# Kernel tuning notes

Measured on AMD Instinct MI355X. Metric: run time of the kernel, lower is better.

The kernel has to match this reference:

```python
import jax, jax.numpy as jnp
import numpy as np

N, E, G = 100000, 800000, 4096
H, F_NODE, F_EDGE, T_OUT = 256, 133, 7, 12
NUM_LAYERS, NUM_TIMESTEPS = 4, 2
SLOPE = 0.01  # negative_slope used throughout AttentiveFP


def _lrelu(v):
    return jax.nn.leaky_relu(v, SLOPE)


def _seg_softmax(logits, seg, n):
    # PyG softmax: exp(x - segment_max) / (segment_sum + 1e-16)
    m = jax.ops.segment_max(logits, seg, num_segments=n)
    e = jnp.exp(logits - m[seg])
    s = jax.ops.segment_sum(e, seg, num_segments=n)
    return e / (s[seg] + 1e-16)


def _gru(xin, h, w_ih, w_hh, b_ih, b_hh):
    # torch.nn.GRUCell, gate order (r, z, n)
    gi = xin @ w_ih.T + b_ih
    gh = h @ w_hh.T + b_hh
    i_r, i_z, i_n = jnp.split(gi, 3, axis=-1)
    h_r, h_z, h_n = jnp.split(gh, 3, axis=-1)
    r = jax.nn.sigmoid(i_r + h_r)
    z = jax.nn.sigmoid(i_z + h_z)
    n = jnp.tanh(i_n + r * h_n)
    return (1.0 - z) * n + z * h


def setup_inputs() -> dict:
    key = jax.random.key(0)
    ks = iter(jax.random.split(key, 40))
    rn = lambda shape, s=0.1: jax.random.normal(next(ks), shape, jnp.float32) * s
    return {
        'x': jax.random.normal(next(ks), (N, F_NODE), jnp.float32),
        'edge_attr': jax.random.normal(next(ks), (E, F_EDGE), jnp.float32),
        'lin1_w': rn((H, F_NODE)), 'lin1_b': rn((H,)),
        'gate_att_l': rn((H,)), 'gate_att_r': rn((H,)),
        'gate_lin1_w': rn((H, H + F_EDGE)), 'gate_lin2_w': rn((H, H)), 'gate_bias': rn((H,)),
        'atom_lin_w': rn((NUM_LAYERS - 1, H, H)), 'atom_att_src': rn((NUM_LAYERS - 1, H)),
        'atom_att_dst': rn((NUM_LAYERS - 1, H)), 'atom_bias': rn((NUM_LAYERS - 1, H)),
        'gru_w_ih': rn((NUM_LAYERS, 3 * H, H)), 'gru_w_hh': rn((NUM_LAYERS, 3 * H, H)),
        'gru_b_ih': rn((NUM_LAYERS, 3 * H)), 'gru_b_hh': rn((NUM_LAYERS, 3 * H)),
        'mol_lin_w': rn((H, H)), 'mol_att_src': rn((H,)), 'mol_att_dst': rn((H,)), 'mol_bias': rn((H,)),
        'mol_gru_w_ih': rn((3 * H, H)), 'mol_gru_w_hh': rn((3 * H, H)),
        'mol_gru_b_ih': rn((3 * H,)), 'mol_gru_b_hh': rn((3 * H,)),
        'lin2_w': rn((H, H)), 'lin2_b': rn((H,)),
        'fc_w': rn((T_OUT, H)), 'fc_b': rn((T_OUT,)),
        'edge_index': jax.random.randint(next(ks), (2, E), 0, N),
        'batch': jnp.sort(jax.random.randint(next(ks), (N,), 0, G)),
        'num_graphs': G,
    }


def reference(x, edge_attr, lin1_w, lin1_b, gate_att_l, gate_att_r, gate_lin1_w,
              gate_lin2_w, gate_bias, atom_lin_w, atom_att_src, atom_att_dst, atom_bias,
              gru_w_ih, gru_w_hh, gru_b_ih, gru_b_hh, mol_lin_w, mol_att_src, mol_att_dst,
              mol_bias, mol_gru_w_ih, mol_gru_w_hh, mol_gru_b_ih, mol_gru_b_hh,
              lin2_w, lin2_b, fc_w, fc_b, edge_index, batch, num_graphs):
    # Eval mode: all dropouts are identity.
    src, dst = edge_index[0], edge_index[1]
    n = x.shape[0]

    x0 = _lrelu(x @ lin1_w.T + lin1_b)  # [N, H]

    # --- GATEConv: edge-feature attention message passing ---
    xj = _lrelu(jnp.concatenate([x0[src], edge_attr], axis=-1) @ gate_lin1_w.T)  # [E, H]
    alpha = _lrelu(xj @ gate_att_l + (x0 @ gate_att_r)[dst])
    alpha = _seg_softmax(alpha, dst, n)
    msg = (x0 @ gate_lin2_w.T)[src] * alpha[:, None]  # [E, H]
    h = jax.ops.segment_sum(msg, dst, num_segments=n) + gate_bias
    xcur = jax.nn.relu(_gru(jax.nn.elu(h), x0, gru_w_ih[0], gru_w_hh[0], gru_b_ih[0], gru_b_hh[0]))

    # --- (num_layers-1) GATConv layers (heads=1, no self loops, slope 0.01) ---
    for l in range(atom_lin_w.shape[0]):
        xl = xcur @ atom_lin_w[l].T  # [N, H]
        a = _lrelu((xl @ atom_att_src[l])[src] + (xl @ atom_att_dst[l])[dst])
        a = _seg_softmax(a, dst, n)
        h = jax.ops.segment_sum(xl[src] * a[:, None], dst, num_segments=n) + atom_bias[l]
        xcur = jax.nn.relu(_gru(jax.nn.elu(h), xcur,
                                gru_w_ih[l + 1], gru_w_hh[l + 1], gru_b_ih[l + 1], gru_b_hh[l + 1]))

    # --- Molecule embedding: attention pooling over node->graph bipartite edges ---
    out = jax.nn.relu(jax.ops.segment_sum(xcur, batch, num_segments=num_graphs))  # [G, H]
    xm = xcur @ mol_lin_w.T              # src transform, fixed across timesteps
    a_src = xm @ mol_att_src             # [N]
    for _ in range(NUM_TIMESTEPS):
        a = _lrelu(a_src + ((out @ mol_lin_w.T) @ mol_att_dst)[batch])
        a = _seg_softmax(a, batch, num_graphs)
        h = jax.ops.segment_sum(xm * a[:, None], batch, num_segments=num_graphs) + mol_bias
        out = jax.nn.relu(_gru(jax.nn.elu(h), out,
                               mol_gru_w_ih, mol_gru_w_hh, mol_gru_b_ih, mol_gru_b_hh))

    emb = out @ lin2_w.T + lin2_b        # AttentiveFP lin2
    return emb @ fc_w.T + fc_b           # [G, num_tasks]
```

## Files before the change

### kernel.cpp

```cpp
#include <hip/hip_runtime.h>
#include <math.h>
#include <stdio.h>
#include <stdint.h>

#define NH 256
#define NH3 768
#define FNODE 133
#define FEDGE 7
#define LDW_GATE1 263
#define NGRAPH 4096
#define NTASK 12
#define SLOPE 0.01f
#define CHUNK 25000
#define PADK 40
#define KPAD_X 160
#define LDC2 512
#define SCAN_TILE 2048

typedef __attribute__((ext_vector_type(4))) float f32x4;
typedef __attribute__((ext_vector_type(8))) _Float16 f16x8;
typedef __attribute__((ext_vector_type(4))) _Float16 f16x4;
typedef __attribute__((ext_vector_type(2))) _Float16 f16x2;

static __device__ __forceinline__ float lrelu_f(float x) { return x > 0.f ? x : SLOPE * x; }
static __device__ __forceinline__ f16x2 lrelu2(f16x2 v) {
    f16x2 z = {(_Float16)0.f, (_Float16)0.f};
    f16x2 s = {(_Float16)SLOPE, (_Float16)SLOPE};
    return __builtin_elementwise_max(v, z) + __builtin_elementwise_min(v, z) * s;
}

template<int ACT, int OB, int AF16>
static __device__ __forceinline__ void gemm_core(
    _Float16* As, _Float16* Ws,
    const void* __restrict__ Av, const float* __restrict__ W,
    const float* __restrict__ bias, const float* __restrict__ bias2,
    void* __restrict__ Cout,
    int M, int K, int Nout, int ldA, int ldW, int ldC, int ocol, int Kw, int bn)
{
    const int bm = blockIdx.y * 64;
    const int tid = threadIdx.x;
    const int wv = tid >> 6, lane = tid & 63;
    const int l15 = lane & 15, l4 = lane >> 4;
    const bool kvec = ((K & 31) == 0) && ((ldA & 3) == 0);
    const bool wvec = ((K & 31) == 0) && ((ldW & 3) == 0) && (Kw == K);
    const int ar = tid >> 2, akq = (tid & 3) * 8;

    f32x4 acc[16];
#pragma unroll
    for (int c = 0; c < 16; ++c) acc[c] = (f32x4){0.f, 0.f, 0.f, 0.f};

    for (int k0 = 0; k0 < K; k0 += 32) {
        {
            const int ga = bm + ar;
            _Float16* dstA = &As[ar * PADK + akq];
            if (AF16) {
                const _Float16* A = (const _Float16*)Av;
                if (ga < M) {
                    *reinterpret_cast<f16x8*>(dstA) =
                        *reinterpret_cast<const f16x8*>(A + (size_t)ga * ldA + k0 + akq);
                } else {
#pragma unroll
                    for (int j = 0; j < 8; ++j) dstA[j] = (_Float16)0.f;
                }
            } else {
                const float* A = (const float*)Av;
                if (ga < M && kvec) {
                    const float4* ap4 = reinterpret_cast<const float4*>(A + (size_t)ga * ldA + k0 + akq);
                    float4 v0 = ap4[0], v1 = ap4[1];
                    dstA[0] = (_Float16)v0.x; dstA[1] = (_Float16)v0.y;
                    dstA[2] = (_Float16)v0.z; dstA[3] = (_Float16)v0.w;
                    dstA[4] = (_Float16)v1.x; dstA[5] = (_Float16)v1.y;
                    dstA[6] = (_Float16)v1.z; dstA[7] = (_Float16)v1.w;
                } else {
                    const float* ap = A + (size_t)ga * ldA + k0 + akq;
#pragma unroll
                    for (int j = 0; j < 8; ++j) {
                        int gk = k0 + akq + j;
                        float v = (ga < M && gk < K) ? ap[j] : 0.f;
                        dstA[j] = (_Float16)v;
                    }
                }
            }
        }
#pragma unroll
        for (int q = 0; q < 4; ++q) {
            const int r = ar + 64 * q;
            const int gw = bn + r;
            _Float16* dstW = &Ws[r * PADK + akq];
            if (gw < Nout && wvec) {
                const float4* wp4 = reinterpret_cast<const float4*>(W + (size_t)gw * ldW + k0 + akq);
                float4 v0 = wp4[0], v1 = wp4[1];
                dstW[0] = (_Float16)v0.x; dstW[1] = (_Float16)v0.y;
                dstW[2] = (_Float16)v0.z; dstW[3] = (_Float16)v0.w;
                dstW[4] = (_Float16)v1.x; dstW[5] = (_Float16)v1.y;
                dstW[6] = (_Float16)v1.z; dstW[7] = (_Float16)v1.w;
            } else {
                const float* wp = W + (size_t)gw * ldW + k0 + akq;
#pragma unroll
                for (int j = 0; j < 8; ++j) {
                    int gk = k0 + akq + j;
                    float v = (gw < Nout && gk < Kw) ? wp[j] : 0.f;
                    dstW[j] = (_Float16)v;
                }
            }
        }
        __syncthreads();
        f16x8 af = *reinterpret_cast<const f16x8*>(&As[(wv * 16 + l15) * PADK + l4 * 8]);
#pragma unroll
        for (int c = 0; c < 16; ++c) {
            f16x8 wf = *reinterpret_cast<const f16x8*>(&Ws[(c * 16 + l15) * PADK + l4 * 8]);
            acc[c] = __builtin_amdgcn_mfma_f32_16x16x32_f16(af, wf, acc[c], 0, 0, 0);
        }
        __syncthreads();
    }

#pragma unroll
    for (int c = 0; c < 16; ++c) {
        int gc = bn + c * 16 + l15;
        if (gc >= Nout) continue;
        float bv = (bias ? bias[gc] : 0.f) + (bias2 ? bias2[gc] : 0.f);
#pragma unroll
        for (int q = 0; q < 4; ++q) {
            int gr = bm + wv * 16 + l4 * 4 + q;
            if (gr >= M) continue;
            float v = acc[c][q] + bv;
            if (ACT == 1) v = lrelu_f(v);
            else if (ACT == 2) v = (v > 0.f ? v : expm1f(v));
            else if (ACT == 3) v = 1.f / (1.f + expf(-v));
            size_t off = (size_t)gr * ldC + ocol + gc;
            if (OB) ((_Float16*)Cout)[off] = (_Float16)v;
            else    ((float*)Cout)[off] = v;
        }
    }
}

template<int ACT, int OB, int AF16>
__global__ __launch_bounds__(256, 4) void gemm_mfma(
    const void* __restrict__ A, const float* __restrict__ W,
    const float* __restrict__ bias, void* __restrict__ Cout,
    int M, int K, int Nout, int ldA, int ldW, int ldC, int ocol, int Kw)
{
    __shared__ _Float16 As[64 * PADK];
    __shared__ _Float16 Ws[256 * PADK];
    gemm_core<ACT, OB, AF16>(As, Ws, A, W, bias, nullptr, Cout,
                             M, K, Nout, ldA, ldW, ldC, ocol, Kw, blockIdx.x * 256);
}

__global__ __launch_bounds__(256, 4) void gemm_gru_a(
    const _Float16* __restrict__ Acat, const float* __restrict__ wcat,
    const float* __restrict__ wih, const float* __restrict__ bih, const float* __restrict__ bhh,
    _Float16* __restrict__ srz, _Float16* __restrict__ innb, int mc)
{
    __shared__ _Float16 As[64 * PADK];
    __shared__ _Float16 Ws[256 * PADK];
    int z = blockIdx.z;
    if (z < 2)
        gemm_core<3, 1, 1>(As, Ws, Acat, wcat, bih, bhh, srz,
                           mc, 512, 512, LDC2, 512, 512, 0, 512, z * 256);
    else
        gemm_core<0, 1, 1>(As, Ws, Acat, wih + 512 * NH, bih + 512, nullptr, innb,
                           mc, NH, NH, LDC2, NH, NH, 0, NH, 0);
}

__global__ __launch_bounds__(256, 4) void gemm_gru_b(
    _Float16* __restrict__ Acat, const float* __restrict__ whh, const float* __restrict__ bhh,
    const _Float16* __restrict__ srz, const _Float16* __restrict__ innb,
    const float* __restrict__ us, const float* __restrict__ ud,
    float* __restrict__ dotr, float* __restrict__ adst, int mc)
{
    __shared__ _Float16 As[64 * PADK];
    __shared__ _Float16 Ws[256 * PADK];
    const float* Wn = whh + 512 * NH;
    const int bm = blockIdx.y * 64;
    const int tid = threadIdx.x;
    const int wv = tid >> 6, lane = tid & 63;
    const int l15 = lane & 15, l4 = lane >> 4;
    const int ar = tid >> 2, akq = (tid & 3) * 8;

    f32x4 acc[16];
#pragma unroll
    for (int c = 0; c < 16; ++c) acc[c] = (f32x4){0.f, 0.f, 0.f, 0.f};

    for (int k0 = 0; k0 < NH; k0 += 32) {
        {
            const int ga = bm + ar;
            _Float16* dstA = &As[ar * PADK + akq];
            if (ga < mc) {
                *reinterpret_cast<f16x8*>(dstA) =
                    *reinterpret_cast<const f16x8*>(Acat + (size_t)ga * LDC2 + NH + k0 + akq);
            } else {
#pragma unroll
                for (int j = 0; j < 8; ++j) dstA[j] = (_Float16)0.f;
            }
        }
#pragma unroll
        for (int q = 0; q < 4; ++q) {
            const int r = ar + 64 * q;
            _Float16* dstW = &Ws[r * PADK + akq];
            const float4* wp4 = reinterpret_cast<const float4*>(Wn + (size_t)r * NH + k0 + akq);
            float4 v0 = wp4[0], v1 = wp4[1];
            dstW[0] = (_Float16)v0.x; dstW[1] = (_Float16)v0.y;
            dstW[2] = (_Float16)v0.z; dstW[3] = (_Float16)v0.w;
            dstW[4] = (_Float16)v1.x; dstW[5] = (_Float16)v1.y;
            dstW[6] = (_Float16)v1.z; dstW[7] = (_Float16)v1.w;
        }
        __syncthreads();
        f16x8 af = *reinterpret_cast<const f16x8*>(&As[(wv * 16 + l15) * PADK + l4 * 8]);
#pragma unroll
        for (int c = 0; c < 16; ++c) {
            f16x8 wf = *reinterpret_cast<const f16x8*>(&Ws[(c * 16 + l15) * PADK + l4 * 8]);
            acc[c] = __builtin_amdgcn_mfma_f32_16x16x32_f16(af, wf, acc[c], 0, 0, 0);
        }
        __syncthreads();
    }

    float pd1[4] = {0.f, 0.f, 0.f, 0.f};
    float pd2[4] = {0.f, 0.f, 0.f, 0.f};
#pragma unroll
    for (int c = 0; c < 16; ++c) {
        int gc = c * 16 + l15;
        float bhn = bhh[512 + gc];
        float usv = us ? us[gc] : 0.f;
        float udv = ud ? ud[gc] : 0.f;
#pragma unroll
        for (int q = 0; q < 4; ++q) {
            int gr = bm + wv * 16 + l4 * 4 + q;
            if (gr >= mc) continue;
            float hn = acc[c][q] + bhn;
            float rr = (float)srz[(size_t)gr * 512 + gc];
            float zz = (float)srz[(size_t)gr * 512 + 256 + gc];
            float inn = (float)innb[(size_t)gr * NH + gc];
            float nn = tanhf(inn + rr * hn);
            size_t xoff = (size_t)gr * LDC2 + NH + gc;
            float xold = (float)Acat[xoff];
            float hv = fmaxf((1.f - zz) * nn + zz * xold, 0.f);
            Acat[xoff] = (_Float16)hv;
            pd1[q] += hv * usv;
            pd2[q] += hv * udv;
        }
    }
    if (us) {
#pragma unroll
        for (int off = 1; off < 16; off <<= 1) {
#pragma unroll
            for (int q = 0; q < 4; ++q) {
                pd1[q] += __shfl_xor(pd1[q], off);
                pd2[q] += __shfl_xor(pd2[q], off);
            }
        }
        if (l15 == 0) {
#pragma unroll
            for (int q = 0; q < 4; ++q) {
                int gr = bm + wv * 16 + l4 * 4 + q;
                if (gr < mc) {
                    dotr[gr] = pd1[q];
                    if (ud) adst[gr] = pd2[q];
                }
            }
        }
    }
}

template<int ACT, int OB>
__global__ __launch_bounds__(256, 4) void gemm_mfma2(
    const float* __restrict__ A0, const float* __restrict__ A1,
    const float* __restrict__ W0, const float* __restrict__ W1,
    void* __restrict__ C0, void* __restrict__ C1, int M, int K, int Nout)
{
    __shared__ _Float16 As[64 * PADK];
    __shared__ _Float16 Ws[256 * PADK];
    int bn = blockIdx.x * 256;
    if (blockIdx.z == 0)
        gemm_core<ACT, OB, 0>(As, Ws, A0, W0, nullptr, nullptr, C0, M, K, Nout, K, K, Nout, 0, K, bn);
    else
        gemm_core<ACT, OB, 0>(As, Ws, A1, W1, nullptr, nullptr, C1, M, K, Nout, K, K, Nout, 0, K, bn);
}

__global__ void build_wcat(const float* __restrict__ wih, const float* __restrict__ whh,
                           float* __restrict__ wcat)
{
    int i = blockIdx.x * 256 + threadIdx.x;
    if (i >= 512 * 512) return;
    int j = i >> 9, k = i & 511;
    wcat[i] = (k < 256) ? wih[j * 256 + k] : whh[j * 256 + (k - 256)];
}

__global__ void pad_cast_f16(const float* __restrict__ in, _Float16* __restrict__ out,
                             int M, int Kin, int Kout)
{
    size_t i = (size_t)blockIdx.x * 256 + threadIdx.x;
    if (i >= (size_t)M * Kout) return;
    int r = (int)(i / Kout), k = (int)(i % Kout);
    out[i] = (k < Kin) ? (_Float16)in[(size_t)r * Kin + k] : (_Float16)0.f;
}

__global__ __launch_bounds__(256) void gemm_nt(
    const float* __restrict__ A, const float* __restrict__ W,
    const float* __restrict__ bias, float* __restrict__ C,
    int M, int K, int Nout, int ldW, int act)
{
    __shared__ float As[16][65];
    __shared__ float Ws[16][65];
    const int bm = blockIdx.y * 64;
    const int bn = blockIdx.x * 64;
    const int tid = threadIdx.x;
    const int tr = tid >> 4, tc = tid & 15;
    const int lrow = tid >> 2, lk = (tid & 3) * 4;
    float acc[4][4] = {};
    for (int k0 = 0; k0 < K; k0 += 16) {
#pragma unroll
        for (int j = 0; j < 4; ++j) {
            int gk = k0 + lk + j;
            int ga = bm + lrow;
            As[lk + j][lrow] = (ga < M && gk < K) ? A[(size_t)ga * K + gk] : 0.f;
            int gw = bn + lrow;
            Ws[lk + j][lrow] = (gw < Nout && gk < K) ? W[(size_t)gw * ldW + gk] : 0.f;
        }
        __syncthreads();
#pragma unroll
        for (int kk = 0; kk < 16; ++kk) {
            float av[4], bv[4];
#pragma unroll
            for (int i = 0; i < 4; ++i) av[i] = As[kk][tr * 4 + i];
#pragma unroll
            for (int i = 0; i < 4; ++i) bv[i] = Ws[kk][tc * 4 + i];
#pragma unroll
            for (int i = 0; i < 4; ++i)
#pragma unroll
                for (int j = 0; j < 4; ++j) acc[i][j] += av[i] * bv[j];
        }
        __syncthreads();
    }
#pragma unroll
    for (int i = 0; i < 4; ++i) {
        int m = bm + tr * 4 + i;
        if (m >= M) continue;
#pragma unroll
        for (int j = 0; j < 4; ++j) {
            int n = bn + tc * 4 + j;
            if (n >= Nout) continue;
            float v = acc[i][j];
            if (bias) v += bias[n];
            if (act == 1) v = lrelu_f(v);
            C[(size_t)m * Nout + n] = v;
        }
    }
}

__global__ void zero_i32(int* p, int n) {
    int i = blockIdx.x * 256 + threadIdx.x;
    if (i < n) p[i] = 0;
}
__global__ void hist_k(const int* __restrict__ key, int* __restrict__ deg, int E) {
    int i = blockIdx.x * 256 + threadIdx.x;
    if (i < E) atomicAdd(&deg[key[i]], 1);
}
__global__ __launch_bounds__(256) void scan_pass1(
    const int* __restrict__ deg, int* __restrict__ bsum, int Nn)
{
    __shared__ int lds[256];
    int b = blockIdx.x, t = threadIdx.x;
    int base = b * SCAN_TILE + t * 8;
    int s = 0;
#pragma unroll
    for (int q = 0; q < 8; ++q) { int i = base + q; if (i < Nn) s += deg[i]; }
    lds[t] = s;
    __syncthreads();
    for (int off = 128; off; off >>= 1) {
        if (t < off) lds[t] += lds[t + off];
        __syncthreads();
    }
    if (t == 0) bsum[b] = lds[0];
}
__global__ __launch_bounds__(256) void scan_pass2(
    const int* __restrict__ bsum, int* __restrict__ boff, int nb, int* __restrict__ total)
{
    __shared__ int lds[256];
    int t = threadIdx.x;
    int v = (t < nb) ? bsum[t] : 0;
    lds[t] = v;
    __syncthreads();
    for (int off = 1; off < 256; off <<= 1) {
        int u = (t >= off) ? lds[t - off] : 0;
        __syncthreads();
        lds[t] += u;
        __syncthreads();
    }
    if (t < nb) boff[t] = lds[t] - v;
    if (t == 255 && total) *total = lds[255];
}
__global__ __launch_bounds__(256) void scan_pass3(
    const int* __restrict__ deg, const int* __restrict__ boff,
    int* __restrict__ rowptr, int* __restrict__ cursor, int Nn)
{
    __shared__ int lds[256];
    int b = blockIdx.x, t = threadIdx.x;
    int base = b * SCAN_TILE + t * 8;
    int v[8];
    int s = 0;
#pragma unroll
    for (int q = 0; q < 8; ++q) { int i = base + q; v[q] = (i < Nn) ? deg[i] : 0; s += v[q]; }
    lds[t] = s;
    __syncthreads();
    for (int off = 1; off < 256; off <<= 1) {
        int u = (t >= off) ? lds[t - off] : 0;
        __syncthreads();
        lds[t] += u;
        __syncthreads();
    }
    int run = boff[b] + lds[t] - s;
#pragma unroll
    for (int q = 0; q < 8; ++q) {
        int i = base + q;
        if (i < Nn) { rowptr[i] = run; cursor[i] = run; run += v[q]; }
    }
}
__global__ void csr_scatter(const int* __restrict__ src, const int* __restrict__ dst,
                            int* __restrict__ cursor, int* __restrict__ esrc,
                            int* __restrict__ pos, int E)
{
    int e = blockIdx.x * 256 + threadIdx.x;
    if (e < E) {
        int p = atomicAdd(&cursor[dst[e]], 1);
        esrc[p] = src[e];
        pos[e] = p;
    }
}
__global__ void csc_scatter(const int* __restrict__ src, int* __restrict__ cursor,
                            int* __restrict__ seid, int E)
{
    int e = blockIdx.x * 256 + threadIdx.x;
    if (e < E) {
        int p = atomicAdd(&cursor[src[e]], 1);
        seid[p] = e;
    }
}
__global__ void edge_csc_build(const float* __restrict__ edge_attr, const int* __restrict__ seid,
// ... 167 lines not shown
    float a0 = 0.f, a1 = 0.f, a2 = 0.f, a3 = 0.f;
    if (beg < end) {
        float dg = ddot[g];
        float m = -3.4e38f;
        for (int i = beg + lane; i < end; i += 64)
            m = fmaxf(m, lrelu_f(dotr[i] + dg));
#pragma unroll
        for (int off = 32; off; off >>= 1) m = fmaxf(m, __shfl_xor(m, off));
        float s = 0.f;
        for (int i = beg + lane; i < end; i += 64)
            s += expf(lrelu_f(dotr[i] + dg) - m);
#pragma unroll
        for (int off = 32; off; off >>= 1) s += __shfl_xor(s, off);
        float inv = 1.f / (s + 1e-16f);
        for (int i = beg; i < end; ++i) {
            float a = expf(lrelu_f(dotr[i] + dg) - m) * inv;
            const _Float16* xr = X + (size_t)i * ldX;
            a0 += a * (float)xr[lane];       a1 += a * (float)xr[64 + lane];
            a2 += a * (float)xr[128 + lane]; a3 += a * (float)xr[192 + lane];
        }
    }
    float* hr = hout + (size_t)g * NH;
    hr[lane] = a0; hr[64 + lane] = a1; hr[128 + lane] = a2; hr[192 + lane] = a3;
}

__global__ __launch_bounds__(256) void graph_sum_relu(
    const _Float16* __restrict__ X, int ldX, const int* __restrict__ gptr,
    float* __restrict__ out, int G)
{
    int wv = threadIdx.x >> 6, lane = threadIdx.x & 63;
    int g = blockIdx.x * 4 + wv;
    if (g >= G) return;
    int beg = gptr[g], end = gptr[g + 1];
    float a0 = 0.f, a1 = 0.f, a2 = 0.f, a3 = 0.f;
    for (int i = beg; i < end; ++i) {
        const _Float16* xr = X + (size_t)i * ldX;
        a0 += (float)xr[lane];       a1 += (float)xr[64 + lane];
        a2 += (float)xr[128 + lane]; a3 += (float)xr[192 + lane];
    }
    float* hr = out + (size_t)g * NH;
    hr[lane] = fmaxf(a0, 0.f); hr[64 + lane] = fmaxf(a1, 0.f);
    hr[128 + lane] = fmaxf(a2, 0.f); hr[192 + lane] = fmaxf(a3, 0.f);
}

template<typename TX>
__global__ __launch_bounds__(256) void node_dot(
    const TX* __restrict__ X, int ldX, const float* __restrict__ v1, const float* __restrict__ v2,
    float* __restrict__ o1, float* __restrict__ o2, int M)
{
    __shared__ float s1[NH], s2[NH];
    int tid = threadIdx.x;
    s1[tid] = v1[tid];
    s2[tid] = v2 ? v2[tid] : 0.f;
    __syncthreads();
    int wv = tid >> 6, lane = tid & 63;
    for (int n = blockIdx.x * 4 + wv; n < M; n += gridDim.x * 4) {
        float a1 = 0.f, a2 = 0.f;
#pragma unroll
        for (int i = 0; i < 4; ++i) {
            int hh = i * 64 + lane;
            float xv = (float)X[(size_t)n * ldX + hh];
            a1 += xv * s1[hh];
            a2 += xv * s2[hh];
        }
#pragma unroll
        for (int off = 32; off; off >>= 1) { a1 += __shfl_xor(a1, off); a2 += __shfl_xor(a2, off); }
        if (lane == 0) { o1[n] = a1; if (o2) o2[n] = a2; }
    }
}

__global__ __launch_bounds__(256) void matvec_left(
    const float* __restrict__ Wm, const float* __restrict__ a, float* __restrict__ v)
{
    int j = threadIdx.x;
    float s = 0.f;
    for (int i = 0; i < NH; ++i) s += a[i] * Wm[(size_t)i * NH + j];
    v[j] = s;
}

__global__ __launch_bounds__(256) void gru_combine(
    const _Float16* __restrict__ gi, const _Float16* __restrict__ gh,
    const float* __restrict__ b_ih, const float* __restrict__ b_hh,
    const float* __restrict__ hprev, float* __restrict__ out, int M)
{
    size_t t = (size_t)blockIdx.x * 256 + threadIdx.x;
    if (t >= (size_t)M * 32) return;
    int n = (int)(t >> 5), j0 = ((int)t & 31) * 8;
    size_t b3 = (size_t)n * NH3;
    f16x8 vir = *reinterpret_cast<const f16x8*>(&gi[b3 + j0]);
    f16x8 viz = *reinterpret_cast<const f16x8*>(&gi[b3 + NH + j0]);
    f16x8 vin = *reinterpret_cast<const f16x8*>(&gi[b3 + 2 * NH + j0]);
    f16x8 vhr = *reinterpret_cast<const f16x8*>(&gh[b3 + j0]);
    f16x8 vhz = *reinterpret_cast<const f16x8*>(&gh[b3 + NH + j0]);
    f16x8 vhn = *reinterpret_cast<const f16x8*>(&gh[b3 + 2 * NH + j0]);
    size_t hb = (size_t)n * NH + j0;
#pragma unroll
    for (int q = 0; q < 8; ++q) {
        int j = j0 + q;
        float r = 1.f / (1.f + expf(-((float)vir[q] + b_ih[j] + (float)vhr[q] + b_hh[j])));
        float z = 1.f / (1.f + expf(-((float)viz[q] + b_ih[NH + j] + (float)vhz[q] + b_hh[NH + j])));
        float nn = tanhf((float)vin[q] + b_ih[2 * NH + j] + r * ((float)vhn[q] + b_hh[2 * NH + j]));
        out[hb + q] = fmaxf((1.f - z) * nn + z * hprev[hb + q], 0.f);
    }
}

extern "C" void kernel_launch(void* const* d_in, const int* in_sizes, int n_in,
                              void* d_out, int out_size, void* d_ws, size_t ws_size,
                              hipStream_t stream)
{
    const float* x          = (const float*)d_in[0];
    const float* edge_attr  = (const float*)d_in[1];
    const float* lin1_w     = (const float*)d_in[2];
    const float* lin1_b     = (const float*)d_in[3];
    const float* gate_att_l = (const float*)d_in[4];
    const float* gate_att_r = (const float*)d_in[5];
    const float* gate_lin1_w= (const float*)d_in[6];
    const float* gate_lin2_w= (const float*)d_in[7];
    const float* gate_bias  = (const float*)d_in[8];
    const float* atom_lin_w = (const float*)d_in[9];
    const float* atom_att_src=(const float*)d_in[10];
    const float* atom_att_dst=(const float*)d_in[11];
    const float* atom_bias  = (const float*)d_in[12];
    const float* gru_w_ih   = (const float*)d_in[13];
    const float* gru_w_hh   = (const float*)d_in[14];
    const float* gru_b_ih   = (const float*)d_in[15];
    const float* gru_b_hh   = (const float*)d_in[16];
    const float* mol_lin_w  = (const float*)d_in[17];
    const float* mol_att_src= (const float*)d_in[18];
    const float* mol_att_dst= (const float*)d_in[19];
    const float* mol_bias   = (const float*)d_in[20];
    const float* mol_gru_w_ih=(const float*)d_in[21];
    const float* mol_gru_w_hh=(const float*)d_in[22];
    const float* mol_gru_b_ih=(const float*)d_in[23];
    const float* mol_gru_b_hh=(const float*)d_in[24];
    const float* lin2_w     = (const float*)d_in[25];
    const float* lin2_b     = (const float*)d_in[26];
    const float* fc_w       = (const float*)d_in[27];
    const float* fc_b       = (const float*)d_in[28];
    const int*   edge_index = (const int*)d_in[29];
    const int*   batch      = (const int*)d_in[30];

    const int N = in_sizes[0] / FNODE;
    const int E = in_sizes[1] / FEDGE;
    const int G = NGRAPH;
    const int* src = edge_index;
    const int* dst = edge_index + E;

    float* w = (float*)d_ws;
    size_t o = 0;
    auto alloc = [&](size_t cnt) { size_t r = o; o += cnt; return r; };
    const size_t o_B1cat = alloc((size_t)N * NH);
    const size_t o_B2    = alloc((size_t)N * NH / 2);
    const size_t o_B3    = alloc((size_t)CHUNK * 512);
    const size_t o_wcat  = alloc((size_t)512 * 512);
    const size_t o_elog  = alloc((size_t)E);
    const size_t o_dotr  = alloc((size_t)N);
    const size_t o_adst  = alloc((size_t)N);
    const size_t o_ddot  = alloc((size_t)G);
    const size_t o_vvec  = alloc((size_t)NH);
    const size_t o_usrc  = alloc((size_t)NH);
    const size_t o_udst  = alloc((size_t)NH);
    const size_t o_rowp  = alloc((size_t)N + 1);
    const size_t o_srowp = alloc((size_t)N + 1);
    const size_t o_deg   = alloc((size_t)N);
    const size_t o_curs  = alloc((size_t)N);
    const size_t o_bsum  = alloc((size_t)512);
    const size_t o_esrc  = alloc((size_t)E);
    const size_t o_pos   = alloc((size_t)E);
    const size_t o_seid  = alloc((size_t)E);
    const size_t o_ecsc  = alloc((size_t)E * 4);
    const size_t o_pcsc  = alloc((size_t)E);
    const size_t o_gptr  = alloc((size_t)G + 1);
    if (o * sizeof(float) > ws_size) {
        fprintf(stderr, "kernel_launch: ws too small: need %zu have %zu\n", o * 4, ws_size);
        return;
    }

    _Float16* B1cat = (_Float16*)(w + o_B1cat);
    _Float16* xcur  = B1cat + NH;
    _Float16* B2 = (_Float16*)(w + o_B2);
    float* B3   = w + o_B3;
    float* wcat = w + o_wcat;
    float* elog = w + o_elog;
    float* dotr = w + o_dotr;
    float* adst = w + o_adst;
    float* ddot = w + o_ddot;
    float* vvec = w + o_vvec;
    float* usrc = w + o_usrc;
    float* udst = w + o_udst;
    int* rowptr  = (int*)(w + o_rowp);
    int* srowptr = (int*)(w + o_srowp);
    int* deg     = (int*)(w + o_deg);
    int* cursor  = (int*)(w + o_curs);
    int* bsum    = (int*)(w + o_bsum);
    int* boff    = bsum + 256;
    int* esrc    = (int*)(w + o_esrc);
    int* pos     = (int*)(w + o_pos);
    int* seid    = (int*)(w + o_seid);
    _Float16* ecsc = (_Float16*)(w + o_ecsc);
    int* pcsc    = (int*)(w + o_pcsc);
    int* gptr    = (int*)(w + o_gptr);

    float* B2f = (float*)B2;
    float*    gout   = B2f;
    float*    hraw_g = B2f + (size_t)G * NH;
    float*    h_g    = B2f + (size_t)2 * G * NH;
    _Float16* gig    = (_Float16*)(B2f + (size_t)3 * G * NH);
    _Float16* ghg    = (_Float16*)(B2f + (size_t)3 * G * NH + (size_t)G * NH3 / 2);
    float*    emb    = B2f + (size_t)3 * G * NH + (size_t)G * NH3;

    const int BLK = 256;
    auto cdiv = [](size_t a, size_t b) { return (int)((a + b - 1) / b); };
    const int gridNodeWave = cdiv(N, 4);
    const int gridEdgeThr = cdiv(E, BLK);
    const int gridNodeThr = cdiv(N, BLK);
    const int CAP = 4096;
    const int gridNodeCap = gridNodeWave < CAP ? gridNodeWave : CAP;
    const int nScanB = cdiv(N, SCAN_TILE);

    auto run_scan = [&](int* rowp) {
        scan_pass1<<<nScanB, BLK, 0, stream>>>(deg, bsum, N);
        scan_pass2<<<1, BLK, 0, stream>>>(bsum, boff, nScanB, rowp + N);
        scan_pass3<<<nScanB, BLK, 0, stream>>>(deg, boff, rowp, cursor, N);
    };

    zero_i32<<<gridNodeThr, BLK, 0, stream>>>(deg, N);
    hist_k<<<gridEdgeThr, BLK, 0, stream>>>(dst, deg, E);
    run_scan(rowptr);
    csr_scatter<<<gridEdgeThr, BLK, 0, stream>>>(src, dst, cursor, esrc, pos, E);
    zero_i32<<<gridNodeThr, BLK, 0, stream>>>(deg, N);
    hist_k<<<gridEdgeThr, BLK, 0, stream>>>(src, deg, E);
    run_scan(srowptr);
    csc_scatter<<<gridEdgeThr, BLK, 0, stream>>>(src, cursor, seid, E);
    edge_csc_build<<<gridEdgeThr, BLK, 0, stream>>>(edge_attr, seid, pos, ecsc, pcsc, E);
    gptr_build<<<cdiv(G + 1, BLK), BLK, 0, stream>>>(batch, gptr, N, G);

    auto run_tail = [&](const float* Wh, const float* bh,
                        const float* wih, const float* whh,
                        const float* bih, const float* bhh,
                        const float* usv, const float* udv) {
        _Float16* innb = (_Float16*)B3;
        _Float16* srz  = innb + (size_t)CHUNK * NH;
        build_wcat<<<1024, BLK, 0, stream>>>(wih, whh, wcat);
        dim3 gFull(1, cdiv(N, 64));
        gemm_mfma<2, 1, 1><<<gFull, BLK, 0, stream>>>(B2, Wh, bh, B1cat,
                                                      N, NH, NH, NH, NH, LDC2, 0, NH);
        for (int c0 = 0; c0 < N; c0 += CHUNK) {
            int mc = (N - c0) < CHUNK ? (N - c0) : CHUNK;
            dim3 gA(1, cdiv(mc, 64), 3);
            gemm_gru_a<<<gA, BLK, 0, stream>>>(B1cat + (size_t)c0 * LDC2, wcat, wih,
                                               bih, bhh, srz, innb, mc);
            dim3 gB(1, cdiv(mc, 64));
            gemm_gru_b<<<gB, BLK, 0, stream>>>(B1cat + (size_t)c0 * LDC2, whh, bhh,
                                               srz, innb, usv, udv, dotr + c0, adst + c0, mc);
        }
    };

    dim3 gridNH(1, cdiv(N, 64));

    _Float16* xpad = (_Float16*)B3;
    pad_cast_f16<<<cdiv((size_t)N * KPAD_X, BLK), BLK, 0, stream>>>(x, xpad, N, FNODE, KPAD_X);
    gemm_mfma<1, 1, 1><<<gridNH, BLK, 0, stream>>>(xpad, lin1_w, lin1_b, B1cat,
                                                   N, KPAD_X, NH, KPAD_X, FNODE, LDC2, NH, FNODE);

    gemm_mfma<0, 1, 1><<<gridNH, BLK, 0, stream>>>(xcur, gate_lin1_w, nullptr, B2,
                                                   N, NH, NH, LDC2, LDW_GATE1, NH, 0, NH);
    node_dot<_Float16><<<gridNodeCap, BLK, 0, stream>>>(xcur, LDC2, gate_att_r, nullptr,
                                                        dotr, nullptr, N);
    gate_part_csc<<<gridNodeCap, BLK, 0, stream>>>(B2, ecsc, gate_lin1_w, gate_att_l,
                                                   srowptr, pcsc, elog, N);
    gate_agg_csr<<<gridNodeWave, BLK, 0, stream>>>(xcur, LDC2, elog, dotr, rowptr, esrc, B2, N);
    matvec_left<<<1, BLK, 0, stream>>>(atom_lin_w, atom_att_src, usrc);
    matvec_left<<<1, BLK, 0, stream>>>(atom_lin_w, atom_att_dst, udst);
    run_tail(gate_lin2_w, gate_bias, gru_w_ih, gru_w_hh, gru_b_ih, gru_b_hh, usrc, udst);

    for (int l = 0; l < 3; ++l) {
        const float* wl = atom_lin_w + (size_t)l * NH * NH;
        gat_agg_csr<<<gridNodeWave, BLK, 0, stream>>>(xcur, LDC2, dotr, adst, rowptr, esrc, B2, N);
        const float* nus = usrc;
        const float* nud = udst;
        if (l < 2) {
            matvec_left<<<1, BLK, 0, stream>>>(atom_lin_w + (size_t)(l + 1) * NH * NH,
                                               atom_att_src + (l + 1) * NH, usrc);
            matvec_left<<<1, BLK, 0, stream>>>(atom_lin_w + (size_t)(l + 1) * NH * NH,
                                               atom_att_dst + (l + 1) * NH, udst);
        } else {
            matvec_left<<<1, BLK, 0, stream>>>(mol_lin_w, mol_att_src, usrc);
            nud = nullptr;
        }
        run_tail(wl, atom_bias + l * NH,
                 gru_w_ih + (size_t)(l + 1) * NH3 * NH, gru_w_hh + (size_t)(l + 1) * NH3 * NH,
                 gru_b_ih + (size_t)(l + 1) * NH3, gru_b_hh + (size_t)(l + 1) * NH3, nus, nud);
    }

    const int gridGWave = cdiv(G, 4);
    graph_sum_relu<<<gridGWave, BLK, 0, stream>>>(xcur, LDC2, gptr, gout, G);
    matvec_left<<<1, BLK, 0, stream>>>(mol_lin_w, mol_att_dst, vvec);

    dim3 gridGH(1, cdiv(G, 64));
    dim3 gridGD(3, cdiv(G, 64), 2);
    for (int t = 0; t < 2; ++t) {
        node_dot<float><<<gridGWave, BLK, 0, stream>>>(gout, NH, vvec, nullptr, ddot, nullptr, G);
        mol_agg_csr<<<gridGWave, BLK, 0, stream>>>(xcur, LDC2, dotr, ddot, gptr, hraw_g, G);
        gemm_mfma<2, 0, 0><<<gridGH, BLK, 0, stream>>>(hraw_g, mol_lin_w, mol_bias, h_g,
                                                       G, NH, NH, NH, NH, NH, 0, NH);
        gemm_mfma2<0, 1><<<gridGD, BLK, 0, stream>>>(h_g, gout, mol_gru_w_ih, mol_gru_w_hh,
                                                     gig, ghg, G, NH, NH3);
        gru_combine<<<cdiv((size_t)G * 32, BLK), BLK, 0, stream>>>(
            gig, ghg, mol_gru_b_ih, mol_gru_b_hh, gout, gout, G);
    }

    gemm_mfma<0, 0, 0><<<gridGH, BLK, 0, stream>>>(gout, lin2_w, lin2_b, emb,
                                                   G, NH, NH, NH, NH, NH, 0, NH);
    dim3 gridFc(1, cdiv(G, 64));
    gemm_nt<<<gridFc, BLK, 0, stream>>>(emb, fc_w, fc_b, (float*)d_out, G, NH, NTASK, NH, 0);
}
```

Before: 3.392 ms.

## Pre-cast GEMM weights to fp16 once and register-prefetch next K tile

All node-level GEMM weights (lin1, gate, atom, GRU) are converted to fp16 once up front. New gemm16 kernels then load fp16 weights directly instead of reading fp32 and converting inside every block on every K step. The new kernels also prefetch the next K tile into registers while MFMAs run on the current shared-memory tile, overlapping global loads with compute. In exchange this adds several small cast launches and about 1MB of workspace, and it drops the Nout/bounds checks, assuming full 256-wide outputs.

```diff
diff --git a/kernel.cpp b/kernel.cpp
--- a/kernel.cpp
+++ b/kernel.cpp
@@ -29,82 +29,42 @@
     return __builtin_elementwise_max(v, z) + __builtin_elementwise_min(v, z) * s;
 }
 
-template<int ACT, int OB, int AF16>
-static __device__ __forceinline__ void gemm_core(
+template<int ACT>
+static __device__ __forceinline__ void gemm16_core(
     _Float16* As, _Float16* Ws,
-    const void* __restrict__ Av, const float* __restrict__ W,
+    const _Float16* __restrict__ A, const _Float16* __restrict__ Wf,
     const float* __restrict__ bias, const float* __restrict__ bias2,
-    void* __restrict__ Cout,
-    int M, int K, int Nout, int ldA, int ldW, int ldC, int ocol, int Kw, int bn)
+    _Float16* __restrict__ Cout,
+    int M, int K, int ldA, int ldC, int ocol)
 {
     const int bm = blockIdx.y * 64;
     const int tid = threadIdx.x;
     const int wv = tid >> 6, lane = tid & 63;
     const int l15 = lane & 15, l4 = lane >> 4;
-    const bool kvec = ((K & 31) == 0) && ((ldA & 3) == 0);
-    const bool wvec = ((K & 31) == 0) && ((ldW & 3) == 0) && (Kw == K);
     const int ar = tid >> 2, akq = (tid & 3) * 8;
+    const int ga = bm + ar;
+
+    f16x8 ra, rw[4];
+    auto loadT = [&](int k0) {
+        if (ga < M) ra = *reinterpret_cast<const f16x8*>(A + (size_t)ga * ldA + k0 + akq);
+        else { f16x8 z = {}; ra = z; }
+#pragma unroll
+        for (int q = 0; q < 4; ++q)
+            rw[q] = *reinterpret_cast<const f16x8*>(Wf + (size_t)(ar + 64 * q) * K + k0 + akq);
+    };
 
     f32x4 acc[16];
 #pragma unroll
     for (int c = 0; c < 16; ++c) acc[c] = (f32x4){0.f, 0.f, 0.f, 0.f};
 
+    loadT(0);
     for (int k0 = 0; k0 < K; k0 += 32) {
-        {
-            const int ga = bm + ar;
-            _Float16* dstA = &As[ar * PADK + akq];
-            if (AF16) {
-                const _Float16* A = (const _Float16*)Av;
-                if (ga < M) {
-                    *reinterpret_cast<f16x8*>(dstA) =
-                        *reinterpret_cast<const f16x8*>(A + (size_t)ga * ldA + k0 + akq);
-                } else {
-#pragma unroll
-                    for (int j = 0; j < 8; ++j) dstA[j] = (_Float16)0.f;
-                }
-            } else {
-                const float* A = (const float*)Av;
-                if (ga < M && kvec) {
-                    const float4* ap4 = reinterpret_cast<const float4*>(A + (size_t)ga * ldA + k0 + akq);
-                    float4 v0 = ap4[0], v1 = ap4[1];
-                    dstA[0] = (_Float16)v0.x; dstA[1] = (_Float16)v0.y;
-                    dstA[2] = (_Float16)v0.z; dstA[3] = (_Float16)v0.w;
-                    dstA[4] = (_Float16)v1.x; dstA[5] = (_Float16)v1.y;
-                    dstA[6] = (_Float16)v1.z; dstA[7] = (_Float16)v1.w;
-                } else {
-                    const float* ap = A + (size_t)ga * ldA + k0 + akq;
-#pragma unroll
-                    for (int j = 0; j < 8; ++j) {
-                        int gk = k0 + akq + j;
-                        float v = (ga < M && gk < K) ? ap[j] : 0.f;
-                        dstA[j] = (_Float16)v;
-                    }
-                }
-            }
-        }
-#pragma unroll
-        for (int q = 0; q < 4; ++q) {
-            const int r = ar + 64 * q;
-            const int gw = bn + r;
-            _Float16* dstW = &Ws[r * PADK + akq];
-            if (gw < Nout && wvec) {
-                const float4* wp4 = reinterpret_cast<const float4*>(W + (size_t)gw * ldW + k0 + akq);
-                float4 v0 = wp4[0], v1 = wp4[1];
-                dstW[0] = (_Float16)v0.x; dstW[1] = (_Float16)v0.y;
-                dstW[2] = (_Float16)v0.z; dstW[3] = (_Float16)v0.w;
-                dstW[4] = (_Float16)v1.x; dstW[5] = (_Float16)v1.y;
-                dstW[6] = (_Float16)v1.z; dstW[7] = (_Float16)v1.w;
-            } else {
-                const float* wp = W + (size_t)gw * ldW + k0 + akq;
-#pragma unroll
-                for (int j = 0; j < 8; ++j) {
-                    int gk = k0 + akq + j;
-                    float v = (gw < Nout && gk < Kw) ? wp[j] : 0.f;
-                    dstW[j] = (_Float16)v;
-                }
-            }
-        }
-        __syncthreads();
+        *reinterpret_cast<f16x8*>(&As[ar * PADK + akq]) = ra;
+#pragma unroll
+        for (int q = 0; q < 4; ++q)
+            *reinterpret_cast<f16x8*>(&Ws[(ar + 64 * q) * PADK + akq]) = rw[q];
+        __syncthreads();
+        if (k0 + 32 < K) loadT(k0 + 32);
         f16x8 af = *reinterpret_cast<const f16x8*>(&As[(wv * 16 + l15) * PADK + l4 * 8]);
 #pragma unroll
         for (int c = 0; c < 16; ++c) {
@@ -116,8 +76,7 @@
 
 #pragma unroll
     for (int c = 0; c < 16; ++c) {
-        int gc = bn + c * 16 + l15;
-        if (gc >= Nout) continue;
+        int gc = c * 16 + l15;
         float bv = (bias ? bias[gc] : 0.f) + (bias2 ? bias2[gc] : 0.f);
 #pragma unroll
         for (int q = 0; q < 4; ++q) {
@@ -127,84 +86,74 @@
             if (ACT == 1) v = lrelu_f(v);
             else if (ACT == 2) v = (v > 0.f ? v : expm1f(v));
             else if (ACT == 3) v = 1.f / (1.f + expf(-v));
-            size_t off = (size_t)gr * ldC + ocol + gc;
-            if (OB) ((_Float16*)Cout)[off] = (_Float16)v;
-            else    ((float*)Cout)[off] = v;
-        }
-    }
-}
-
-template<int ACT, int OB, int AF16>
-__global__ __launch_bounds__(256, 4) void gemm_mfma(
-    const void* __restrict__ A, const float* __restrict__ W,
-    const float* __restrict__ bias, void* __restrict__ Cout,
-    int M, int K, int Nout, int ldA, int ldW, int ldC, int ocol, int Kw)
+            Cout[(size_t)gr * ldC + ocol + gc] = (_Float16)v;
+        }
+    }
+}
+
+template<int ACT>
+__global__ __launch_bounds__(256, 4) void gemm16(
+    const _Float16* __restrict__ A, const _Float16* __restrict__ Wf,
+    const float* __restrict__ bias, _Float16* __restrict__ Cout,
+    int M, int K, int ldA, int ldC, int ocol)
 {
     __shared__ _Float16 As[64 * PADK];
     __shared__ _Float16 Ws[256 * PADK];
-    gemm_core<ACT, OB, AF16>(As, Ws, A, W, bias, nullptr, Cout,
-                             M, K, Nout, ldA, ldW, ldC, ocol, Kw, blockIdx.x * 256);
-}
-
-__global__ __launch_bounds__(256, 4) void gemm_gru_a(
-    const _Float16* __restrict__ Acat, const float* __restrict__ wcat,
-    const float* __restrict__ wih, const float* __restrict__ bih, const float* __restrict__ bhh,
+    gemm16_core<ACT>(As, Ws, A, Wf, bias, nullptr, Cout, M, K, ldA, ldC, ocol);
+}
+
+__global__ __launch_bounds__(256, 4) void gemm_gru_a16(
+    const _Float16* __restrict__ Acat, const _Float16* __restrict__ wcat16,
+    const _Float16* __restrict__ wihn16,
+    const float* __restrict__ bih, const float* __restrict__ bhh,
     _Float16* __restrict__ srz, _Float16* __restrict__ innb, int mc)
 {
     __shared__ _Float16 As[64 * PADK];
     __shared__ _Float16 Ws[256 * PADK];
     int z = blockIdx.z;
     if (z < 2)
-        gemm_core<3, 1, 1>(As, Ws, Acat, wcat, bih, bhh, srz,
-                           mc, 512, 512, LDC2, 512, 512, 0, 512, z * 256);
+        gemm16_core<3>(As, Ws, Acat, wcat16 + (size_t)z * 256 * 512, bih + z * 256, bhh + z * 256,
+                       srz, mc, 512, LDC2, 512, z * 256);
     else
-        gemm_core<0, 1, 1>(As, Ws, Acat, wih + 512 * NH, bih + 512, nullptr, innb,
-                           mc, NH, NH, LDC2, NH, NH, 0, NH, 0);
-}
-
-__global__ __launch_bounds__(256, 4) void gemm_gru_b(
-    _Float16* __restrict__ Acat, const float* __restrict__ whh, const float* __restrict__ bhh,
+        gemm16_core<0>(As, Ws, Acat, wihn16, bih + 512, nullptr, innb, mc, 256, LDC2, 256, 0);
+}
+
+__global__ __launch_bounds__(256, 4) void gemm_gru_b16(
+    _Float16* __restrict__ Acat, const _Float16* __restrict__ Wn16, const float* __restrict__ bhh,
     const _Float16* __restrict__ srz, const _Float16* __restrict__ innb,
     const float* __restrict__ us, const float* __restrict__ ud,
     float* __restrict__ dotr, float* __restrict__ adst, int mc)
 {
     __shared__ _Float16 As[64 * PADK];
     __shared__ _Float16 Ws[256 * PADK];
-    const float* Wn = whh + 512 * NH;
     const int bm = blockIdx.y * 64;
     const int tid = threadIdx.x;
     const int wv = tid >> 6, lane = tid & 63;
     const int l15 = lane & 15, l4 = lane >> 4;
     const int ar = tid >> 2, akq = (tid & 3) * 8;
+    const int ga = bm + ar;
+
+    f16x8 ra, rw[4];
+    auto loadT = [&](int k0) {
+        if (ga < mc) ra = *reinterpret_cast<const f16x8*>(Acat + (size_t)ga * LDC2 + NH + k0 + akq);
+        else { f16x8 z = {}; ra = z; }
+#pragma unroll
+        for (int q = 0; q < 4; ++q)
+            rw[q] = *reinterpret_cast<const f16x8*>(Wn16 + (size_t)(ar + 64 * q) * NH + k0 + akq);
+    };
 
     f32x4 acc[16];
 #pragma unroll
     for (int c = 0; c < 16; ++c) acc[c] = (f32x4){0.f, 0.f, 0.f, 0.f};
 
+    loadT(0);
     for (int k0 = 0; k0 < NH; k0 += 32) {
-        {
-            const int ga = bm + ar;
-            _Float16* dstA = &As[ar * PADK + akq];
-            if (ga < mc) {
-                *reinterpret_cast<f16x8*>(dstA) =
-                    *reinterpret_cast<const f16x8*>(Acat + (size_t)ga * LDC2 + NH + k0 + akq);
-            } else {
-#pragma unroll
-                for (int j = 0; j < 8; ++j) dstA[j] = (_Float16)0.f;
-            }
-        }
-#pragma unroll
-        for (int q = 0; q < 4; ++q) {
-            const int r = ar + 64 * q;
-            _Float16* dstW = &Ws[r * PADK + akq];
-            const float4* wp4 = reinterpret_cast<const float4*>(Wn + (size_t)r * NH + k0 + akq);
-            float4 v0 = wp4[0], v1 = wp4[1];
-            dstW[0] = (_Float16)v0.x; dstW[1] = (_Float16)v0.y;
-            dstW[2] = (_Float16)v0.z; dstW[3] = (_Float16)v0.w;
-            dstW[4] = (_Float16)v1.x; dstW[5] = (_Float16)v1.y;
-            dstW[6] = (_Float16)v1.z; dstW[7] = (_Float16)v1.w;
-        }
-        __syncthreads();
+        *reinterpret_cast<f16x8*>(&As[ar * PADK + akq]) = ra;
+#pragma unroll
+        for (int q = 0; q < 4; ++q)
+            *reinterpret_cast<f16x8*>(&Ws[(ar + 64 * q) * PADK + akq]) = rw[q];
+        __syncthreads();
+        if (k0 + 32 < NH) loadT(k0 + 32);
         f16x8 af = *reinterpret_cast<const f16x8*>(&As[(wv * 16 + l15) * PADK + l4 * 8]);
 #pragma unroll
         for (int c = 0; c < 16; ++c) {
@@ -261,6 +210,121 @@
     }
 }
 
+template<int ACT, int OB, int AF16>
+static __device__ __forceinline__ void gemm_core(
+    _Float16* As, _Float16* Ws,
+    const void* __restrict__ Av, const float* __restrict__ W,
+    const float* __restrict__ bias, void* __restrict__ Cout,
+    int M, int K, int Nout, int ldA, int ldW, int ldC, int ocol, int Kw, int bn)
+{
+    const int bm = blockIdx.y * 64;
+    const int tid = threadIdx.x;
+    const int wv = tid >> 6, lane = tid & 63;
+    const int l15 = lane & 15, l4 = lane >> 4;
+    const bool kvec = ((K & 31) == 0) && ((ldA & 3) == 0);
+    const bool wvec = ((K & 31) == 0) && ((ldW & 3) == 0) && (Kw == K);
+    const int ar = tid >> 2, akq = (tid & 3) * 8;
+
+    f32x4 acc[16];
+#pragma unroll
+    for (int c = 0; c < 16; ++c) acc[c] = (f32x4){0.f, 0.f, 0.f, 0.f};
+
+    for (int k0 = 0; k0 < K; k0 += 32) {
+        {
+            const int ga = bm + ar;
+            _Float16* dstA = &As[ar * PADK + akq];
+            if (AF16) {
+                const _Float16* A = (const _Float16*)Av;
+                if (ga < M) {
+                    *reinterpret_cast<f16x8*>(dstA) =
+                        *reinterpret_cast<const f16x8*>(A + (size_t)ga * ldA + k0 + akq);
+                } else {
+#pragma unroll
+                    for (int j = 0; j < 8; ++j) dstA[j] = (_Float16)0.f;
+                }
+            } else {
+                const float* A = (const float*)Av;
+                if (ga < M && kvec) {
+                    const float4* ap4 = reinterpret_cast<const float4*>(A + (size_t)ga * ldA + k0 + akq);
+                    float4 v0 = ap4[0], v1 = ap4[1];
+                    dstA[0] = (_Float16)v0.x; dstA[1] = (_Float16)v0.y;
+                    dstA[2] = (_Float16)v0.z; dstA[3] = (_Float16)v0.w;
+                    dstA[4] = (_Float16)v1.x; dstA[5] = (_Float16)v1.y;
+                    dstA[6] = (_Float16)v1.z; dstA[7] = (_Float16)v1.w;
+                } else {
+                    const float* ap = A + (size_t)ga * ldA + k0 + akq;
+#pragma unroll
+                    for (int j = 0; j < 8; ++j) {
+                        int gk = k0 + akq + j;
+                        float v = (ga < M && gk < K) ? ap[j] : 0.f;
+                        dstA[j] = (_Float16)v;
+                    }
+                }
+            }
+        }
+#pragma unroll
+        for (int q = 0; q < 4; ++q) {
+            const int r = ar + 64 * q;
+            const int gw = bn + r;
+            _Float16* dstW = &Ws[r * PADK + akq];
+            if (gw < Nout && wvec) {
+                const float4* wp4 = reinterpret_cast<const float4*>(W + (size_t)gw * ldW + k0 + akq);
+                float4 v0 = wp4[0], v1 = wp4[1];
+                dstW[0] = (_Float16)v0.x; dstW[1] = (_Float16)v0.y;
+                dstW[2] = (_Float16)v0.z; dstW[3] = (_Float16)v0.w;
+                dstW[4] = (_Float16)v1.x; dstW[5] = (_Float16)v1.y;
+                dstW[6] = (_Float16)v1.z; dstW[7] = (_Float16)v1.w;
+            } else {
+                const float* wp = W + (size_t)gw * ldW + k0 + akq;
+#pragma unroll
+                for (int j = 0; j < 8; ++j) {
+                    int gk = k0 + akq + j;
+                    float v = (gw < Nout && gk < Kw) ? wp[j] : 0.f;
+                    dstW[j] = (_Float16)v;
+                }
+            }
+        }
+        __syncthreads();
+        f16x8 af = *reinterpret_cast<const f16x8*>(&As[(wv * 16 + l15) * PADK + l4 * 8]);
+#pragma unroll
+        for (int c = 0; c < 16; ++c) {
+            f16x8 wf = *reinterpret_cast<const f16x8*>(&Ws[(c * 16 + l15) * PADK + l4 * 8]);
+            acc[c] = __builtin_amdgcn_mfma_f32_16x16x32_f16(af, wf, acc[c], 0, 0, 0);
+        }
+        __syncthreads();
+    }
+
+#pragma unroll
+    for (int c = 0; c < 16; ++c) {
+        int gc = bn + c * 16 + l15;
+        if (gc >= Nout) continue;
+        float bv = bias ? bias[gc] : 0.f;
+#pragma unroll
+        for (int q = 0; q < 4; ++q) {
+            int gr = bm + wv * 16 + l4 * 4 + q;
+            if (gr >= M) continue;
+            float v = acc[c][q] + bv;
+            if (ACT == 1) v = lrelu_f(v);
+            else if (ACT == 2) v = (v > 0.f ? v : expm1f(v));
+            size_t off = (size_t)gr * ldC + ocol + gc;
+            if (OB) ((_Float16*)Cout)[off] = (_Float16)v;
+            else    ((float*)Cout)[off] = v;
+        }
+    }
+}
+
+template<int ACT, int OB, int AF16>
+__global__ __launch_bounds__(256, 4) void gemm_mfma(
+    const void* __restrict__ A, const float* __restrict__ W,
+    const float* __restrict__ bias, void* __restrict__ Cout,
+    int M, int K, int Nout, int ldA, int ldW, int ldC, int ocol, int Kw)
+{
+    __shared__ _Float16 As[64 * PADK];
+    __shared__ _Float16 Ws[256 * PADK];
+    gemm_core<ACT, OB, AF16>(As, Ws, A, W, bias, Cout, M, K, Nout, ldA, ldW, ldC, ocol, Kw,
+                             blockIdx.x * 256);
+}
+
 template<int ACT, int OB>
 __global__ __launch_bounds__(256, 4) void gemm_mfma2(
     const float* __restrict__ A0, const float* __restrict__ A1,
@@ -271,18 +335,26 @@
     __shared__ _Float16 Ws[256 * PADK];
     int bn = blockIdx.x * 256;
     if (blockIdx.z == 0)
-        gemm_core<ACT, OB, 0>(As, Ws, A0, W0, nullptr, nullptr, C0, M, K, Nout, K, K, Nout, 0, K, bn);
+        gemm_core<ACT, OB, 0>(As, Ws, A0, W0, nullptr, C0, M, K, Nout, K, K, Nout, 0, K, bn);
     else
-        gemm_core<ACT, OB, 0>(As, Ws, A1, W1, nullptr, nullptr, C1, M, K, Nout, K, K, Nout, 0, K, bn);
-}
-
-__global__ void build_wcat(const float* __restrict__ wih, const float* __restrict__ whh,
-                           float* __restrict__ wcat)
+        gemm_core<ACT, OB, 0>(As, Ws, A1, W1, nullptr, C1, M, K, Nout, K, K, Nout, 0, K, bn);
+}
+
+__global__ void cast_w16(const float* __restrict__ src, _Float16* __restrict__ dst,
+                         int rows, int cols, int ldsrc, int kout)
+{
+    int i = blockIdx.x * 256 + threadIdx.x;
+    if (i >= rows * kout) return;
+    int r = i / kout, k = i % kout;
+    dst[i] = (k < cols) ? (_Float16)src[(size_t)r * ldsrc + k] : (_Float16)0.f;
+}
+__global__ void build_wcat16(const float* __restrict__ wih, const float* __restrict__ whh,
+                             _Float16* __restrict__ dst)
 {
     int i = blockIdx.x * 256 + threadIdx.x;
     if (i >= 512 * 512) return;
     int j = i >> 9, k = i & 511;
-    wcat[i] = (k < 256) ? wih[j * 256 + k] : whh[j * 256 + (k - 256)];
+    dst[i] = (_Float16)((k < 256) ? wih[j * 256 + k] : whh[j * 256 + (k - 256)]);
 }
 
 __global__ void pad_cast_f16(const float* __restrict__ in, _Float16* __restrict__ out,
@@ -756,7 +828,7 @@
     const size_t o_B1cat = alloc((size_t)N * NH);
     const size_t o_B2    = alloc((size_t)N * NH / 2);
     const size_t o_B3    = alloc((size_t)CHUNK * 512);
-    const size_t o_wcat  = alloc((size_t)512 * 512);
+    const size_t o_w16   = alloc((size_t)972000);
     const size_t o_elog  = alloc((size_t)E);
     const size_t o_dotr  = alloc((size_t)N);
     const size_t o_adst  = alloc((size_t)N);
@@ -784,7 +856,14 @@
     _Float16* xcur  = B1cat + NH;
     _Float16* B2 = (_Float16*)(w + o_B2);
     float* B3   = w + o_B3;
-    float* wcat = w + o_wcat;
+    _Float16* w16 = (_Float16*)(w + o_w16);
+    _Float16* lin116   = w16;
+    _Float16* gate1a16 = lin116 + 40960;
+    _Float16* gate216  = gate1a16 + 65536;
+    _Float16* atom16   = gate216 + 65536;
+    _Float16* wihn16   = atom16 + 3 * 65536;
+    _Float16* whhn16   = wihn16 + 4 * 65536;
+    _Float16* wcat16   = whhn16 + 4 * 65536;
     float* elog = w + o_elog;
     float* dotr = w + o_dotr;
     float* adst = w + o_adst;
@@ -828,6 +907,22 @@
         scan_pass3<<<nScanB, BLK, 0, stream>>>(deg, boff, rowp, cursor, N);
     };
 
+    cast_w16<<<cdiv(256 * 160, BLK), BLK, 0, stream>>>(lin1_w, lin116, 256, FNODE, FNODE, 160);
+    cast_w16<<<cdiv(65536, BLK), BLK, 0, stream>>>(gate_lin1_w, gate1a16, 256, 256, LDW_GATE1, 256);
+    cast_w16<<<cdiv(65536, BLK), BLK, 0, stream>>>(gate_lin2_w, gate216, 256, 256, 256, 256);
+    for (int l = 0; l < 3; ++l)
+        cast_w16<<<cdiv(65536, BLK), BLK, 0, stream>>>(atom_lin_w + (size_t)l * 65536,
+                                                       atom16 + (size_t)l * 65536, 256, 256, 256, 256);
+    for (int l = 0; l < 4; ++l) {
+        const float* wih = gru_w_ih + (size_t)l * NH3 * NH;
+        const float* whh = gru_w_hh + (size_t)l * NH3 * NH;
+        build_wcat16<<<1024, BLK, 0, stream>>>(wih, whh, wcat16 + (size_t)l * 262144);
+        cast_w16<<<cdiv(65536, BLK), BLK, 0, stream>>>(wih + 512 * NH, wihn16 + (size_t)l * 65536,
+                                                       256, 256, 256, 256);
+        cast_w16<<<cdiv(65536, BLK), BLK, 0, stream>>>(whh + 512 * NH, whhn16 + (size_t)l * 65536,
+                                                       256, 256, 256, 256);
+    }
+
     zero_i32<<<gridNodeThr, BLK, 0, stream>>>(deg, N);
     hist_k<<<gridEdgeThr, BLK, 0, stream>>>(dst, deg, E);
     run_scan(rowptr);
@@ -839,24 +934,24 @@
     edge_csc_build<<<gridEdgeThr, BLK, 0, stream>>>(edge_attr, seid, pos, ecsc, pcsc, E);
     gptr_build<<<cdiv(G + 1, BLK), BLK, 0, stream>>>(batch, gptr, N, G);
 
-    auto run_tail = [&](const float* Wh, const float* bh,
-                        const float* wih, const float* whh,
+    auto run_tail = [&](const _Float16* Wh16, const float* bh, int l,
                         const float* bih, const float* bhh,
                         const float* usv, const float* udv) {
         _Float16* innb = (_Float16*)B3;
         _Float16* srz  = innb + (size_t)CHUNK * NH;
-        build_wcat<<<1024, BLK, 0, stream>>>(wih, whh, wcat);
         dim3 gFull(1, cdiv(N, 64));
-        gemm_mfma<2, 1, 1><<<gFull, BLK, 0, stream>>>(B2, Wh, bh, B1cat,
-                                                      N, NH, NH, NH, NH, LDC2, 0, NH);
+        gemm16<2><<<gFull, BLK, 0, stream>>>(B2, Wh16, bh, B1cat, N, NH, NH, LDC2, 0);
         for (int c0 = 0; c0 < N; c0 += CHUNK) {
             int mc = (N - c0) < CHUNK ? (N - c0) : CHUNK;
             dim3 gA(1, cdiv(mc, 64), 3);
-            gemm_gru_a<<<gA, BLK, 0, stream>>>(B1cat + (size_t)c0 * LDC2, wcat, wih,
-                                               bih, bhh, srz, innb, mc);
+            gemm_gru_a16<<<gA, BLK, 0, stream>>>(B1cat + (size_t)c0 * LDC2,
+                                                 wcat16 + (size_t)l * 262144,
+                                                 wihn16 + (size_t)l * 65536,
+                                                 bih, bhh, srz, innb, mc);
             dim3 gB(1, cdiv(mc, 64));
-            gemm_gru_b<<<gB, BLK, 0, stream>>>(B1cat + (size_t)c0 * LDC2, whh, bhh,
-                                               srz, innb, usv, udv, dotr + c0, adst + c0, mc);
+            gemm_gru_b16<<<gB, BLK, 0, stream>>>(B1cat + (size_t)c0 * LDC2,
+                                                 whhn16 + (size_t)l * 65536, bhh,
+                                                 srz, innb, usv, udv, dotr + c0, adst + c0, mc);
         }
     };
 
@@ -864,11 +959,9 @@
 
     _Float16* xpad = (_Float16*)B3;
     pad_cast_f16<<<cdiv((size_t)N * KPAD_X, BLK), BLK, 0, stream>>>(x, xpad, N, FNODE, KPAD_X);
-    gemm_mfma<1, 1, 1><<<gridNH, BLK, 0, stream>>>(xpad, lin1_w, lin1_b, B1cat,
-                                                   N, KPAD_X, NH, KPAD_X, FNODE, LDC2, NH, FNODE);
-
-    gemm_mfma<0, 1, 1><<<gridNH, BLK, 0, stream>>>(xcur, gate_lin1_w, nullptr, B2,
-                                                   N, NH, NH, LDC2, LDW_GATE1, NH, 0, NH);
+    gemm16<1><<<gridNH, BLK, 0, stream>>>(xpad, lin116, lin1_b, B1cat, N, KPAD_X, KPAD_X, LDC2, NH);
+
+    gemm16<0><<<gridNH, BLK, 0, stream>>>(xcur, gate1a16, nullptr, B2, N, NH, LDC2, NH, 0);
     node_dot<_Float16><<<gridNodeCap, BLK, 0, stream>>>(xcur, LDC2, gate_att_r, nullptr,
                                                         dotr, nullptr, N);
     gate_part_csc<<<gridNodeCap, BLK, 0, stream>>>(B2, ecsc, gate_lin1_w, gate_att_l,
@@ -876,10 +969,9 @@
     gate_agg_csr<<<gridNodeWave, BLK, 0, stream>>>(xcur, LDC2, elog, dotr, rowptr, esrc, B2, N);
     matvec_left<<<1, BLK, 0, stream>>>(atom_lin_w, atom_att_src, usrc);
     matvec_left<<<1, BLK, 0, stream>>>(atom_lin_w, atom_att_dst, udst);
-    run_tail(gate_lin2_w, gate_bias, gru_w_ih, gru_w_hh, gru_b_ih, gru_b_hh, usrc, udst);
+    run_tail(gate216, gate_bias, 0, gru_b_ih, gru_b_hh, usrc, udst);
 
     for (int l = 0; l < 3; ++l) {
-        const float* wl = atom_lin_w + (size_t)l * NH * NH;
         gat_agg_csr<<<gridNodeWave, BLK, 0, stream>>>(xcur, LDC2, dotr, adst, rowptr, esrc, B2, N);
         const float* nus = usrc;
         const float* nud = udst;
@@ -892,8 +984,7 @@
             matvec_left<<<1, BLK, 0, stream>>>(mol_lin_w, mol_att_src, usrc);
             nud = nullptr;
         }
-        run_tail(wl, atom_bias + l * NH,
-                 gru_w_ih + (size_t)(l + 1) * NH3 * NH, gru_w_hh + (size_t)(l + 1) * NH3 * NH,
+        run_tail(atom16 + (size_t)l * 65536, atom_bias + l * NH, l + 1,
                  gru_b_ih + (size_t)(l + 1) * NH3, gru_b_hh + (size_t)(l + 1) * NH3, nus, nud);
     }
 
```

New measurement: 2.979 ms. 1.14x faster.
